# Kernel optimization log

Hardware: AMD Instinct MI355X
Metric: run time of the kernel (lower is better)

The kernel has to match this reference:

```python
import jax, jax.numpy as jnp
from jax import lax
import numpy as np

B, S, T = 32, 512, 64
IN, H, L, HC, OUT = 512, 512, 2, 4, 512

def setup_inputs() -> dict:
    key = jax.random.key(0)
    ks = jax.random.split(key, 12)
    def w(k, shape, fan_in):
        return (jax.random.normal(k, shape, jnp.float32) / np.float32(np.sqrt(fan_in)))
    lstm_in0 = IN + HC * H
    return {
        "inputs": jax.random.normal(ks[0], (B, T, IN), jnp.float32),
        "lengths": jax.random.randint(ks[1], (B,), 1, S + 1),
        "final_hiddens": jax.random.normal(ks[2], (L, B, H), jnp.float32),
        "hiddens": jax.random.normal(ks[3], (B, S, H), jnp.float32),
        "max_output_len": T,
        "max_seq_len": S,
        "Wa1": w(ks[4], (H, 2 * H), 2 * H), "ba1": jnp.zeros((H,), jnp.float32),
        "Wa2": w(ks[5], (HC, H), H), "ba2": jnp.zeros((HC,), jnp.float32),
        "W_ih0": w(ks[6], (4 * H, lstm_in0), lstm_in0), "W_hh0": w(ks[7], (4 * H, H), H),
        "b_ih0": jnp.zeros((4 * H,), jnp.float32), "b_hh0": jnp.zeros((4 * H,), jnp.float32),
        "W_ih1": w(ks[8], (4 * H, H), H), "W_hh1": w(ks[9], (4 * H, H), H),
        "b_ih1": jnp.zeros((4 * H,), jnp.float32), "b_hh1": jnp.zeros((4 * H,), jnp.float32),
        "Wo1": w(ks[10], (H, (1 + HC) * H), (1 + HC) * H), "bo1": jnp.zeros((H,), jnp.float32),
        "Wo2": w(ks[11], (OUT, H), H), "bo2": jnp.zeros((OUT,), jnp.float32),
    }

def _lstm_cell(x, h, c, W_ih, W_hh, b_ih, b_hh):
    # PyTorch LSTM gate order: i, f, g, o
    g = x @ W_ih.T + b_ih + h @ W_hh.T + b_hh
    i, f, gg, o = jnp.split(g, 4, axis=-1)
    c_new = jax.nn.sigmoid(f) * c + jax.nn.sigmoid(i) * jnp.tanh(gg)
    h_new = jax.nn.sigmoid(o) * jnp.tanh(c_new)
    return h_new, c_new

def reference(inputs, lengths, final_hiddens, hiddens, max_output_len, max_seq_len,
              Wa1, ba1, Wa2, ba2, W_ih0, W_hh0, b_ih0, b_hh0,
              W_ih1, W_hh1, b_ih1, b_hh1, Wo1, bo1, Wo2, bo2):
    batch = inputs.shape[0]
    # r_mask[b, s] = 1 if s < lengths[b] else 0  -> [B, S, 1]
    r_mask = (jnp.arange(max_seq_len)[None, :] < lengths[:, None]).astype(hiddens.dtype)[..., None]

    def step(carry, x_t):
        h, c = carry  # each [L, B, H]
        last = h[-1]  # [B, H]
        dup = last[:, None, :] * r_mask  # [B, S, H]
        a = jax.nn.relu(jnp.concatenate([dup, hiddens], axis=2) @ Wa1.T + ba1)  # [B,S,H]
        a = jax.nn.relu(a @ Wa2.T + ba2)  # [B,S,HC]
        a = jax.nn.softmax(a, axis=1)  # softmax over seq dim (unmasked, as in source)
        c_vecs = jnp.einsum('bsk,bsh->bkh', a, hiddens).reshape(batch, -1)  # [B, HC*H]
        x = jnp.concatenate([x_t, c_vecs], axis=1)  # [B, IN + HC*H]
        h0, c0 = _lstm_cell(x, h[0], c[0], W_ih0, W_hh0, b_ih0, b_hh0)
        h1, c1 = _lstm_cell(h0, h[1], c[1], W_ih1, W_hh1, b_ih1, b_hh1)
        out = jnp.tanh(jax.nn.relu(jnp.concatenate([h1, c_vecs], axis=1) @ Wo1.T + bo1) @ Wo2.T + bo2)
        return (jnp.stack([h0, h1]), jnp.stack([c0, c1])), out

    c_init = jnp.zeros_like(final_hiddens)
    _, outs = lax.scan(step, (final_hiddens, c_init), jnp.swapaxes(inputs, 0, 1))  # [T,B,OUT]
    return jnp.swapaxes(outs, 0, 1)  # [B, T, OUT]
```

## Files before the change

kernel.cpp:

```cpp
#include <hip/hip_runtime.h>
#include <cmath>


typedef unsigned short ushort;
typedef unsigned int uint;
typedef __attribute__((ext_vector_type(8))) short bf16x8;
typedef __attribute__((ext_vector_type(4))) float f32x4;

__device__ __forceinline__ float sigmoidf_(float x) { return 1.f / (1.f + __expf(-x)); }
__device__ __forceinline__ float bf2f(ushort u) {
  union { uint i; float f; } x; x.i = ((uint)u) << 16; return x.f;
}
__device__ __forceinline__ ushort f2bf(float f) {
  union { float f; uint i; } x; x.f = f;
  return (ushort)((x.i + 0x7FFFu + ((x.i >> 16) & 1u)) >> 16);
}
__device__ __forceinline__ float wave_sum(float v) {
#pragma unroll
  for (int m = 1; m < 64; m <<= 1) v += __shfl_xor(v, m, 64);
  return v;
}
__device__ __forceinline__ float wave_max(float v) {
#pragma unroll
  for (int m = 1; m < 64; m <<= 1) v = fmaxf(v, __shfl_xor(v, m, 64));
  return v;
}

__global__ void __launch_bounds__(256) k_init(const float* __restrict__ fh,
                                              ushort* h0b0, ushort* h1b0,
                                              float* c0, float* c1) {
  int i = blockIdx.x * 256 + threadIdx.x;
  h0b0[i] = f2bf(fh[i]);
  h1b0[i] = f2bf(fh[16384 + i]);
  c0[i] = 0.f; c1[i] = 0.f;
}

__global__ void __launch_bounds__(256) k_prep(const float* __restrict__ hid,
                                              ushort* __restrict__ hbf) {
  size_t i0 = ((size_t)blockIdx.x * 256 + threadIdx.x) * 8;
  float4 f0 = *(const float4*)&hid[i0];
  float4 f1 = *(const float4*)&hid[i0 + 4];
  uint4 o;
  o.x = (uint)f2bf(f0.x) | ((uint)f2bf(f0.y) << 16);
  o.y = (uint)f2bf(f0.z) | ((uint)f2bf(f0.w) << 16);
  o.z = (uint)f2bf(f1.x) | ((uint)f2bf(f1.y) << 16);
  o.w = (uint)f2bf(f1.z) | ((uint)f2bf(f1.w) << 16);
  *(uint4*)&hbf[i0] = o;
}

__global__ void __launch_bounds__(256) k_inprep(const float* __restrict__ inputs,
                                                ushort* __restrict__ inb) {
  size_t idx4 = ((size_t)blockIdx.x * 256 + threadIdx.x) * 4;
  int m = (int)(idx4 >> 9), k = (int)(idx4 & 511);
  int b = m & 31, tt = m >> 5;
  float4 v = *(const float4*)&inputs[((size_t)b * 64 + tt) * 512 + k];
  ushort4 o; o.x = f2bf(v.x); o.y = f2bf(v.y); o.z = f2bf(v.z); o.w = f2bf(v.w);
  *(ushort4*)&inb[(size_t)m * 512 + k] = o;
}

__global__ void __launch_bounds__(256) k_wcvt(const float* __restrict__ W1, int ld1,
                                              const float* __restrict__ W2, int ld2,
                                              int split, int K,
                                              ushort* __restrict__ dst) {
  size_t idx = ((size_t)blockIdx.x * 256 + threadIdx.x) * 4;
  int j = (int)(idx / K), k = (int)(idx % K);
  const float* src = (k < split) ? (W1 + (size_t)j * ld1 + k)
                                 : (W2 + (size_t)j * ld2 + (k - split));
  float4 v = *(const float4*)src;
  ushort4 o; o.x = f2bf(v.x); o.y = f2bf(v.y); o.z = f2bf(v.z); o.w = f2bf(v.w);
  *(ushort4*)&dst[idx] = o;
}

__device__ __forceinline__ void mfma_slice(
    const ushort* __restrict__ W, int ldW, int jrow0, int jstride,
    const ushort* __restrict__ xA, int ldA, int xsplit,
    const ushort* __restrict__ xB, int ldB, int coff,
    int klo, int khi, float* __restrict__ redrow) {
  const int l = threadIdx.x & 63;
  const int r16 = l & 15, koff = (l >> 4) * 8;
  const int j = jrow0 + (r16 & 3) + (r16 >> 2) * jstride;
  const ushort* wrow = W + (size_t)j * ldW + koff;
  const ushort* a0A = xA + (size_t)r16 * ldA + koff;
  const ushort* a1A = xA + (size_t)(16 + r16) * ldA + koff;
  const ushort* a0B = xB + (size_t)r16 * ldB + koff;
  const ushort* a1B = xB + (size_t)(16 + r16) * ldB + koff;
  f32x4 acc0 = {0.f, 0.f, 0.f, 0.f}, acc1 = {0.f, 0.f, 0.f, 0.f};
#pragma unroll 4
  for (int k0 = klo; k0 < khi; k0 += 32) {
    bf16x8 av0, av1;
    if (k0 < xsplit) {
      av0 = *(const bf16x8*)(a0A + k0);
      av1 = *(const bf16x8*)(a1A + k0);
    } else {
      av0 = *(const bf16x8*)(a0B + (k0 - coff));
      av1 = *(const bf16x8*)(a1B + (k0 - coff));
    }
    bf16x8 wv = *(const bf16x8*)(wrow + k0);
    acc0 = __builtin_amdgcn_mfma_f32_16x16x32_bf16(av0, wv, acc0, 0, 0, 0);
    acc1 = __builtin_amdgcn_mfma_f32_16x16x32_bf16(av1, wv, acc1, 0, 0, 0);
  }
  const int brow = (l >> 4) << 2;
#pragma unroll
  for (int r = 0; r < 4; r++) {
    redrow[r16 * 33 + brow + r] = acc0[r];
    redrow[r16 * 33 + 16 + brow + r] = acc1[r];
  }
}

__global__ void __launch_bounds__(256) k_hidproj2(const ushort* __restrict__ Wa1c,
                                                  const ushort* __restrict__ hbf,
                                                  ushort* __restrict__ hpb) {
  __shared__ float red[4 * 528];
  int tid = threadIdx.x, w = tid >> 6;
  int j0 = blockIdx.x * 16;
  for (int mt = 0; mt < 4; mt++) {
    int m0 = (blockIdx.y * 4 + mt) * 32;
    mfma_slice(Wa1c, 512, j0, 4, hbf + (size_t)m0 * 512, 512, 1 << 30,
               hbf + (size_t)m0 * 512, 512, 0, w * 128, w * 128 + 128,
               red + w * 528);
    __syncthreads();
#pragma unroll
    for (int e = 0; e < 2; e++) {
      int idx = tid + e * 256;
      int j = idx >> 5, b = idx & 31;
      float v = 0.f;
#pragma unroll
      for (int ww = 0; ww < 4; ww++) v += red[ww * 528 + j * 33 + b];
      hpb[(size_t)(m0 + b) * 512 + j0 + j] = f2bf(v);
    }
    __syncthreads();
  }
}

__global__ void __launch_bounds__(512) k_scst(const ushort* __restrict__ hpb,
                                              const float* __restrict__ ba1,
                                              const float* __restrict__ Wa2,
                                              float4* __restrict__ scoresP4) {
  __shared__ float wa2s[256], ba1s[64];
  int bid = blockIdx.x, tid = threadIdx.x;
  int b = bid >> 3, kdq = bid & 7, kd0 = kdq << 6, s = tid;
  if (tid < 256) wa2s[tid] = Wa2[(tid >> 6) * 512 + kd0 + (tid & 63)];
  else if (tid < 320) ba1s[tid - 256] = ba1[kd0 + (tid - 256)];
  __syncthreads();
  float a0 = 0.f, a1 = 0.f, a2 = 0.f, a3 = 0.f;
  const ushort* hpr = hpb + (size_t)(b * 512 + s) * 512 + kd0;
#pragma unroll
  for (int i8 = 0; i8 < 8; i8++) {
    bf16x8 hv8 = *(const bf16x8*)(hpr + i8 * 8);
#pragma unroll
    for (int e = 0; e < 8; e++) {
      int i = i8 * 8 + e;
      float a = fmaxf(bf2f(((ushort*)&hv8)[e]) + ba1s[i], 0.f);
      a0 += wa2s[i] * a;
      a1 += wa2s[64 + i] * a;
      a2 += wa2s[128 + i] * a;
      a3 += wa2s[192 + i] * a;
    }
  }
  scoresP4[((size_t)(kdq * 32 + b)) * 512 + s] = make_float4(a0, a1, a2, a3);
}

__global__ void __launch_bounds__(512) k_sum0(const float4* __restrict__ scoresP4,
                                              const float* __restrict__ ba2,
                                              float* __restrict__ scores0) {
  int idx = blockIdx.x * 512 + threadIdx.x;
  int b = idx >> 9, s = idx & 511;
  float a0 = ba2[0], a1 = ba2[1], a2 = ba2[2], a3 = ba2[3];
#pragma unroll
  for (int q = 0; q < 8; q++) {
    float4 p = scoresP4[((size_t)(q * 32 + b)) * 512 + s];
    a0 += p.x; a1 += p.y; a2 += p.z; a3 += p.w;
  }
  scores0[((size_t)b * 4 + 0) * 512 + s] = fmaxf(a0, 0.f);
  scores0[((size_t)b * 4 + 1) * 512 + s] = fmaxf(a1, 0.f);
  scores0[((size_t)b * 4 + 2) * 512 + s] = fmaxf(a2, 0.f);
  scores0[((size_t)b * 4 + 3) * 512 + s] = fmaxf(a3, 0.f);
}

__global__ void __launch_bounds__(512) k_stat0(const float* __restrict__ scores0,
                                               const int* __restrict__ lengths,
                                               float* __restrict__ m0v,
                                               float* __restrict__ statZ,
                                               float* __restrict__ P0) {
  __shared__ float st[32], st2[32];
  int b = blockIdx.x, tid = threadIdx.x, lane = tid & 63, w = tid >> 6;
  int s = tid, len = lengths[b];
  bool stat = s >= len;
  float v[4], m0[4];
#pragma unroll
  for (int k = 0; k < 4; k++) v[k] = scores0[((size_t)b * 4 + k) * 512 + s];
#pragma unroll
  for (int k = 0; k < 4; k++) {
    float mk = wave_max(stat ? v[k] : -1e30f);
    if (lane == 0) st[w * 4 + k] = mk;
  }
  __syncthreads();
#pragma unroll
  for (int k = 0; k < 4; k++) {
    float m = st[k];
#pragma unroll
    for (int w2 = 1; w2 < 8; w2++) m = fmaxf(m, st[w2 * 4 + k]);
    m0[k] = m;
  }
  float e[4];
#pragma unroll
  for (int k = 0; k < 4; k++) {
    e[k] = stat ? __expf(v[k] - m0[k]) : 0.f;
    float sk = wave_sum(e[k]);
    if (lane == 0) st2[w * 4 + k] = sk;
  }
  __syncthreads();
#pragma unroll
  for (int k = 0; k < 4; k++) {
    P0[((size_t)b * 4 + k) * 512 + s] = e[k];
  }
  if (tid == 0) {
#pragma unroll
    for (int k = 0; k < 4; k++) {
      float z = 0.f;
#pragma unroll
      for (int w2 = 0; w2 < 8; w2++) z += st2[w2 * 4 + k];
      m0v[b * 4 + k] = m0[k];
      statZ[b * 4 + k] = z;
    }
  }
}

__global__ void __launch_bounds__(512) k_statvec(const float* __restrict__ P0,
                                                 const ushort* __restrict__ hbf,
                                                 const int* __restrict__ lengths,
                                                 float* __restrict__ statvec) {
  __shared__ float P[4 * 512];
  __shared__ float red2[8 * 256];
  int bid = blockIdx.x, tid = threadIdx.x;
  int b = bid >> 3, hs = bid & 7;
#pragma unroll
  for (int k = 0; k < 4; k++) P[k * 512 + tid] = P0[((size_t)b * 4 + k) * 512 + tid];
  __syncthreads();
  int h = tid & 63, w8 = tid >> 6;
  int len = lengths[b];
  float a0 = 0.f, a1 = 0.f, a2 = 0.f, a3 = 0.f;
  for (int si = len + ((w8 - len) & 7); si < 512; si += 8) {
    float hv = bf2f(hbf[((size_t)(b * 512 + si) * 512) + (hs << 6) + h]);
    a0 += P[si] * hv;
    a1 += P[512 + si] * hv;
    a2 += P[1024 + si] * hv;
    a3 += P[1536 + si] * hv;
  }
  red2[(w8 << 8) + h] = a0;
  red2[(w8 << 8) + 64 + h] = a1;
  red2[(w8 << 8) + 128 + h] = a2;
  red2[(w8 << 8) + 192 + h] = a3;
  __syncthreads();
  if (tid < 256) {
    int k = tid >> 6, hh = tid & 63;
    float acc = 0.f;
#pragma unroll
    for (int c = 0; c < 8; c++) acc += red2[(c << 8) + (k << 6) + hh];
    statvec[((size_t)b * 4 + k) * 512 + (hs << 6) + hh] = acc;
  }
}

__global__ void __launch_bounds__(256) k_gin0(const ushort* __restrict__ Wg0b,
                                              const ushort* __restrict__ inb,
                                              float* __restrict__ gi0) {
  __shared__ float red[4 * 528];
  int tid = threadIdx.x, w = tid >> 6;
  int j0 = blockIdx.x * 16;
  for (int mt = 0; mt < 4; mt++) {
    int m0 = (blockIdx.y * 4 + mt) * 32;
    mfma_slice(Wg0b, 3072, j0, 4, inb + (size_t)m0 * 512, 512, 1 << 30,
               inb + (size_t)m0 * 512, 512, 0, w * 128, w * 128 + 128,
               red + w * 528);
    __syncthreads();
#pragma unroll
    for (int e = 0; e < 2; e++) {
      int idx = tid + e * 256;
      int j = idx >> 5, b = idx & 31;
      float v = 0.f;
#pragma unroll
      for (int ww = 0; ww < 4; ww++) v += red[ww * 528 + j * 33 + b];
      gi0[(size_t)(m0 + b) * 2048 + j0 + j] = v;
    }
    __syncthreads();
  }
}

__global__ void __launch_bounds__(512) k_scq(
    const ushort* __restrict__ Wq, const ushort* __restrict__ Wo1,
    const ushort* __restrict__ h1cur, const ushort* __restrict__ xb,
    const float* __restrict__ bo1, ushort* __restrict__ o1bf,
    const ushort* __restrict__ hpb, const float* __restrict__ ba1,
    const float* __restrict__ Wa2, const int* __restrict__ lengths,
    float4* __restrict__ scoresP4, int t) {
  __shared__ float red[8 * 528];
  __shared__ float qs[64], wa2s[256], ba1s[64];
  int bid = blockIdx.x, tid = threadIdx.x, w = tid >> 6, lane = tid & 63;
  if (bid < 32) {
    if (t < 1) return;
    mfma_slice(Wo1, 2560, bid * 16, 4, h1cur, 512, 512, xb, 2048, 512,
               w * 320, w * 320 + 320, red + w * 528);
    __syncthreads();
    int j = tid & 15, b = tid >> 4;
    float v = 0.f;
#pragma unroll
    for (int ww = 0; ww < 8; ww++) v += red[ww * 528 + j * 33 + b];
    int jj = bid * 16 + j;
    o1bf[b * 512 + jj] = f2bf(fmaxf(v + bo1[jj], 0.f));
  } else {
    if (t >= 64) return;
    int r = bid - 32;
    int b = r >> 3, kdq = r & 7, kd0 = kdq << 6;
    if (tid < 256) wa2s[tid] = Wa2[(tid >> 6) * 512 + kd0 + (tid & 63)];
    else if (tid < 320) ba1s[tid - 256] = ba1[kd0 + (tid - 256)];
    {
      bf16x8 hv8 = *(const bf16x8*)(h1cur + b * 512 + lane * 8);
      float hf[8];
#pragma unroll
      for (int e2 = 0; e2 < 8; e2++) hf[e2] = bf2f(((ushort*)&hv8)[e2]);
#pragma unroll
      for (int rr = 0; rr < 8; rr++) {
        int row = kd0 + w * 8 + rr;
        bf16x8 wv8 = *(const bf16x8*)(Wq + (size_t)row * 512 + lane * 8);
        float acc = 0.f;
#pragma unroll
        for (int e2 = 0; e2 < 8; e2++) acc += hf[e2] * bf2f(((ushort*)&wv8)[e2]);
        acc = wave_sum(acc);
        if (lane == 0) qs[w * 8 + rr] = acc;
      }
    }
    __syncthreads();
    int s = tid, len = lengths[b];
    if ((tid & ~63) >= len) return;
    float m = (s < len) ? 1.f : 0.f;
    float a0 = 0.f, a1 = 0.f, a2 = 0.f, a3 = 0.f;
    const ushort* hpr = hpb + (size_t)(b * 512 + s) * 512 + kd0;
#pragma unroll
    for (int i8 = 0; i8 < 8; i8++) {
      bf16x8 hv8 = *(const bf16x8*)(hpr + i8 * 8);
#pragma unroll
      for (int e = 0; e < 8; e++) {
        int i = i8 * 8 + e;
        float a = fmaxf(bf2f(((ushort*)&hv8)[e]) + ba1s[i] + m * qs[i], 0.f);
        a0 += wa2s[i] * a;
        a1 += wa2s[64 + i] * a;
        a2 += wa2s[128 + i] * a;
        a3 += wa2s[192 + i] * a;
      }
    }
    scoresP4[((size_t)(kdq * 32 + b)) * 512 + s] = make_float4(a0, a1, a2, a3);
  }
}

__global__ void __launch_bounds__(512) k_ctxout(
    const float4* __restrict__ scoresP4, const float* __restrict__ ba2,
    const int* __restrict__ lengths, const ushort* __restrict__ hbf,
    const float* __restrict__ m0v, const float* __restrict__ statZ,
    const float* __restrict__ statvec, ushort* __restrict__ xb,
    const ushort* __restrict__ Wo2, const ushort* __restrict__ o1bf,
    const float* __restrict__ bo2, float* __restrict__ outp, int t) {
  __shared__ float red[8 * 528];
  __shared__ float P[4 * 512];
  __shared__ float red2[8 * 256];
  __shared__ float st[32], st2[32];
  int bid = blockIdx.x, tid = threadIdx.x;
  if (bid < 32) {
    if (t < 1) return;
    int w = tid >> 6;
    mfma_slice(Wo2, 512, bid * 16, 4, o1bf, 512, 1 << 30, o1bf, 512, 0,
               w * 64, w * 64 + 64, red + w * 528);
    __syncthreads();
    int j = tid & 15, b = tid >> 4;
    float v = 0.f;
#pragma unroll
    for (int ww = 0; ww < 8; ww++) v += red[ww * 528 + j * 33 + b];
    int jj = bid * 16 + j;
    outp[((size_t)b * 64 + (t - 1)) * 512 + jj] = tanhf(v + bo2[jj]);
  } else {
    if (t >= 64) return;
    int r = bid - 32;
    int b = r >> 3, hs = r & 7;
    int lane = tid & 63, w = tid >> 6;
    int s = tid, len = lengths[b];
    bool act = s < len;
    float v[4];
    {
      float a0 = ba2[0], a1 = ba2[1], a2 = ba2[2], a3 = ba2[3];
      if (act) {
#pragma unroll
        for (int q = 0; q < 8; q++) {
          float4 p = scoresP4[((size_t)(q * 32 + b)) * 512 + s];
          a0 += p.x; a1 += p.y; a2 += p.z; a3 += p.w;
        }
        v[0] = fmaxf(a0, 0.f); v[1] = fmaxf(a1, 0.f);
        v[2] = fmaxf(a2, 0.f); v[3] = fmaxf(a3, 0.f);
      } else {
        v[0] = v[1] = v[2] = v[3] = -1e30f;
      }
    }
    float M[4];
#pragma unroll
    for (int k = 0; k < 4; k++) {
      float mk = wave_max(v[k]);
      if (lane == 0) st[w * 4 + k] = mk;
    }
    __syncthreads();
#pragma unroll
    for (int k = 0; k < 4; k++) {
      float m = st[k];
#pragma unroll
      for (int w2 = 1; w2 < 8; w2++) m = fmaxf(m, st[w2 * 4 + k]);
      M[k] = fmaxf(m, m0v[b * 4 + k]);
    }
    float e[4];
#pragma unroll
    for (int k = 0; k < 4; k++) {
      e[k] = act ? __expf(v[k] - M[k]) : 0.f;
      float sk = wave_sum(e[k]);
      if (lane == 0) st2[w * 4 + k] = sk;
    }
    __syncthreads();
    float sc[4];
#pragma unroll
    for (int k = 0; k < 4; k++) {
      float dynZ = 0.f;
#pragma unroll
      for (int w2 = 0; w2 < 8; w2++) dynZ += st2[w2 * 4 + k];
      float scB = __expf(m0v[b * 4 + k] - M[k]);
      float Z = dynZ + scB * statZ[b * 4 + k];
      float invZ = 1.f / Z;
      P[k * 512 + s] = e[k] * invZ;
      sc[k] = scB * invZ;
    }
    __syncthreads();
    int h = tid & 63, w8 = tid >> 6;
    float a0 = 0.f, a1 = 0.f, a2 = 0.f, a3 = 0.f;
    const ushort* hb0 = hbf + ((size_t)b * 512) * 512 + (hs << 6) + h;
    int si = w8;
    for (; si + 24 < len; si += 32) {
      float h0v = bf2f(hb0[(size_t)si * 512]);
      float h1v = bf2f(hb0[(size_t)(si + 8) * 512]);
      float h2v = bf2f(hb0[(size_t)(si + 16) * 512]);
      float h3v = bf2f(hb0[(size_t)(si + 24) * 512]);
      a0 += P[si] * h0v + P[si + 8] * h1v + P[si + 16] * h2v + P[si + 24] * h3v;
      a1 += P[512 + si] * h0v + P[512 + si + 8] * h1v + P[512 + si + 16] * h2v +
            P[512 + si + 24] * h3v;
      a2 += P[1024 + si] * h0v + P[1024 + si + 8] * h1v + P[1024 + si + 16] * h2v +
            P[1024 + si + 24] * h3v;
      a3 += P[1536 + si] * h0v + P[1536 + si + 8] * h1v + P[1536 + si + 16] * h2v +
            P[1536 + si + 24] * h3v;
    }
    for (; si < len; si += 8) {
      float hv = bf2f(hb0[(size_t)si * 512]);
      a0 += P[si] * hv;
      a1 += P[512 + si] * hv;
      a2 += P[1024 + si] * hv;
      a3 += P[1536 + si] * hv;
    }
    red2[(w8 << 8) + h] = a0;
    red2[(w8 << 8) + 64 + h] = a1;
    red2[(w8 << 8) + 128 + h] = a2;
    red2[(w8 << 8) + 192 + h] = a3;
    __syncthreads();
    if (tid < 256) {
      int k = tid >> 6, hh = tid & 63;
      float acc = 0.f;
#pragma unroll
      for (int c = 0; c < 8; c++) acc += red2[(c << 8) + (k << 6) + hh];
      acc += sc[k] * statvec[((size_t)b * 4 + k) * 512 + (hs << 6) + hh];
      xb[b * 2048 + (k << 9) + (hs << 6) + hh] = f2bf(acc);
    }
  }
}

__global__ void __launch_bounds__(512) k_cell0(
    const ushort* __restrict__ Wg0b, const ushort* __restrict__ xb,
    const ushort* __restrict__ h0cur, const float* __restrict__ gi0,
    const float* __restrict__ bih, const float* __restrict__ bhh,
    float* __restrict__ cst, ushort* __restrict__ hnew, int t) {
  __shared__ float red[8 * 528];
  int bid = blockIdx.x, tid = threadIdx.x, w = tid >> 6;
  mfma_slice(Wg0b + 512, 3072, bid * 4, 512, xb, 2048, 2048, h0cur, 512, 2048,
             w * 320, w * 320 + 320, red + w * 528);
  __syncthreads();
  if (tid < 128) {
    int b = tid & 31, dh = tid >> 5;
    int h = bid * 4 + dh;
    float G[4];
#pragma unroll
    for (int g = 0; g < 4; g++) {
      float v = bih[g * 512 + h] + bhh[g * 512 + h] +
                gi0[(size_t)(t * 32 + b) * 2048 + g * 512 + h];
#pragma unroll
      for (int ww = 0; ww < 8; ww++) v += red[ww * 528 + (g * 4 + dh) * 33 + b];
      G[g] = v;
    }
    float i_ = sigmoidf_(G[0]), f_ = sigmoidf_(G[1]);
    float gg = tanhf(G[2]), o_ = sigmoidf_(G[3]);
    float cn = f_ * cst[b * 512 + h] + i_ * gg;
    cst[b * 512 + h] = cn;
    hnew[b * 512 + h] = f2bf(o_ * tanhf(cn));
  }
}

__global__ void __launch_bounds__(512) k_cell1(
    const ushort* __restrict__ Wg1b, const ushort* __restrict__ h0new,
    const ushort* __restrict__ h1cur, const float* __restrict__ bih,
    const float* __restrict__ bhh, float* __restrict__ cst,
    ushort* __restrict__ hnew) {
  __shared__ float red[8 * 528];
  int bid = blockIdx.x, tid = threadIdx.x, w = tid >> 6;
  mfma_slice(Wg1b, 1024, bid * 4, 512, h0new, 512, 512, h1cur, 512, 512,
             w * 128, w * 128 + 128, red + w * 528);
  __syncthreads();
  if (tid < 128) {
    int b = tid & 31, dh = tid >> 5;
    int h = bid * 4 + dh;
    float G[4];
#pragma unroll
    for (int g = 0; g < 4; g++) {
      float v = bih[g * 512 + h] + bhh[g * 512 + h];
#pragma unroll
      for (int ww = 0; ww < 8; ww++) v += red[ww * 528 + (g * 4 + dh) * 33 + b];
      G[g] = v;
    }
    float i_ = sigmoidf_(G[0]), f_ = sigmoidf_(G[1]);
    float gg = tanhf(G[2]), o_ = sigmoidf_(G[3]);
    float cn = f_ * cst[b * 512 + h] + i_ * gg;
    cst[b * 512 + h] = cn;
    hnew[b * 512 + h] = f2bf(o_ * tanhf(cn));
  }
}

extern "C" void kernel_launch(void* const* d_in, const int* in_sizes, int n_in,
                              void* d_out, int out_size, void* d_ws, size_t ws_size,
                              hipStream_t stream) {
  const float* inputs  = (const float*)d_in[0];
  const int*   lengths = (const int*)d_in[1];
  const float* fh      = (const float*)d_in[2];
  const float* hiddens = (const float*)d_in[3];
  const float* Wa1  = (const float*)d_in[6];
  const float* ba1  = (const float*)d_in[7];
  const float* Wa2  = (const float*)d_in[8];
  const float* ba2  = (const float*)d_in[9];
  const float* Wih0 = (const float*)d_in[10];
  const float* Whh0 = (const float*)d_in[11];
  const float* bih0 = (const float*)d_in[12];
  const float* bhh0 = (const float*)d_in[13];
  const float* Wih1 = (const float*)d_in[14];
  const float* Whh1 = (const float*)d_in[15];
  const float* bih1 = (const float*)d_in[16];
  const float* bhh1 = (const float*)d_in[17];
  const float* Wo1  = (const float*)d_in[18];
  const float* bo1  = (const float*)d_in[19];
  const float* Wo2  = (const float*)d_in[20];
  const float* bo2  = (const float*)d_in[21];
  float* outp = (float*)d_out;

  char* p = (char*)d_ws;
  ushort* hpb = (ushort*)p; p += (size_t)32 * 512 * 512 * 2;
  ushort* hbf = (ushort*)p; p += (size_t)32 * 512 * 512 * 2;
  float4* scoresP4 = (float4*)p; p += (size_t)8 * 32 * 512 * 16;
  float* scores0 = (float*)p; p += (size_t)32 * 4 * 512 * 4;
  float* P0      = (float*)p; p += (size_t)32 * 4 * 512 * 4;
  float* statvec = (float*)p; p += (size_t)32 * 4 * 512 * 4;
  float* m0v     = (float*)p; p += 128 * sizeof(float);
  float* statZ   = (float*)p; p += 128 * sizeof(float);
  ushort* xb     = (ushort*)p; p += (size_t)32 * 2048 * 2;
  ushort* h0b    = (ushort*)p; p += (size_t)2 * 32 * 512 * 2;
  ushort* h1b    = (ushort*)p; p += (size_t)2 * 32 * 512 * 2;
  ushort* o1bf   = (ushort*)p; p += (size_t)32 * 512 * 2;
  float* c0      = (float*)p; p += (size_t)32 * 512 * 4;
  float* c1      = (float*)p; p += (size_t)32 * 512 * 4;
  ushort* Wg0b   = (ushort*)p; p += (size_t)2048 * 3072 * 2;
  ushort* Wg1b   = (ushort*)p; p += (size_t)2048 * 1024 * 2;
  ushort* Wo1b   = (ushort*)p; p += (size_t)512 * 2560 * 2;
  ushort* Wo2b   = (ushort*)p; p += (size_t)512 * 512 * 2;
  ushort* Wqb    = (ushort*)p; p += (size_t)512 * 512 * 2;
  ushort* Wa1c   = (ushort*)p; p += (size_t)512 * 512 * 2;
  ushort* inb    = (ushort*)p; p += (size_t)2048 * 512 * 2;
  float* gi0     = (float*)p; p += (size_t)2048 * 2048 * 4;

  k_init<<<64, 256, 0, stream>>>(fh, h0b, h1b, c0, c1);
  k_prep<<<4096, 256, 0, stream>>>(hiddens, hbf);
  k_inprep<<<1024, 256, 0, stream>>>(inputs, inb);
  k_wcvt<<<6144, 256, 0, stream>>>(Wih0, 2560, Whh0, 512, 2560, 3072, Wg0b);
  k_wcvt<<<2048, 256, 0, stream>>>(Wih1, 512, Whh1, 512, 512, 1024, Wg1b);
  k_wcvt<<<1280, 256, 0, stream>>>(Wo1, 2560, Wo1, 2560, 2560, 2560, Wo1b);
  k_wcvt<<<256, 256, 0, stream>>>(Wo2, 512, Wo2, 512, 512, 512, Wo2b);
  k_wcvt<<<256, 256, 0, stream>>>(Wa1, 1024, Wa1, 1024, 512, 512, Wqb);
  k_wcvt<<<256, 256, 0, stream>>>(Wa1 + 512, 1024, Wa1 + 512, 1024, 1 << 30, 512, Wa1c);
  k_hidproj2<<<dim3(32, 128), 256, 0, stream>>>(Wa1c, hbf, hpb);
  k_gin0<<<dim3(128, 16), 256, 0, stream>>>(Wg0b, inb, gi0);
  k_scst<<<256, 512, 0, stream>>>(hpb, ba1, Wa2, scoresP4);
  k_sum0<<<32, 512, 0, stream>>>(scoresP4, ba2, scores0);
  k_stat0<<<32, 512, 0, stream>>>(scores0, lengths, m0v, statZ, P0);
  k_statvec<<<256, 512, 0, stream>>>(P0, hbf, lengths, statvec);

  for (int t = 0; t <= 64; t++) {
    const ushort* h1cur = h1b + (size_t)(t & 1) * 16384;
    const ushort* h0cur = h0b + (size_t)(t & 1) * 16384;
    ushort* h0nxt = h0b + (size_t)((t + 1) & 1) * 16384;
    ushort* h1nxt = h1b + (size_t)((t + 1) & 1) * 16384;
    k_scq<<<288, 512, 0, stream>>>(Wqb, Wo1b, h1cur, xb, bo1, o1bf, hpb, ba1,
                                   Wa2, lengths, scoresP4, t);
    k_ctxout<<<288, 512, 0, stream>>>(scoresP4, ba2, lengths, hbf, m0v, statZ,
                                      statvec, xb, Wo2b, o1bf, bo2, outp, t);
    if (t < 64) {
      k_cell0<<<128, 512, 0, stream>>>(Wg0b, xb, h0cur, gi0, bih0, bhh0, c0,
                                       h0nxt, t);
      k_cell1<<<128, 512, 0, stream>>>(Wg1b, h0nxt, h1cur, bih1, bhh1, c1, h1nxt);
    }
  }
}
```

Before: 2.913 ms.

## Precompute recurrent h@W_hh gate terms in earlier kernels to shorten cell critical path

The recurrent W_hh·h contributions for both LSTM layers are moved out of the cell kernels. They now run as extra blocks in k_scq (layer 1) and k_ctxout (layer 0), which already have h available, and are written to gh0/gh1 buffers that the cell kernels read. This shrinks the serial GEMM work inside k_cell0/k_cell1. Separately, the attention score partitioning changes from 8 to 4 slices of 128 features, which halves the partial-sum traffic but doubles the per-block work. The extra blocks add launch width and global round-trips for the gate partials.

```diff
diff --git a/kernel.cpp b/kernel.cpp
--- a/kernel.cpp
+++ b/kernel.cpp
@@ -136,25 +136,25 @@
                                               const float* __restrict__ ba1,
                                               const float* __restrict__ Wa2,
                                               float4* __restrict__ scoresP4) {
-  __shared__ float wa2s[256], ba1s[64];
+  __shared__ float wa2s[512], ba1s[128];
   int bid = blockIdx.x, tid = threadIdx.x;
-  int b = bid >> 3, kdq = bid & 7, kd0 = kdq << 6, s = tid;
-  if (tid < 256) wa2s[tid] = Wa2[(tid >> 6) * 512 + kd0 + (tid & 63)];
-  else if (tid < 320) ba1s[tid - 256] = ba1[kd0 + (tid - 256)];
+  int b = bid >> 2, kdq = bid & 3, kd0 = kdq << 7, s = tid;
+  wa2s[tid] = Wa2[(tid >> 7) * 512 + kd0 + (tid & 127)];
+  if (tid < 128) ba1s[tid] = ba1[kd0 + tid];
   __syncthreads();
   float a0 = 0.f, a1 = 0.f, a2 = 0.f, a3 = 0.f;
   const ushort* hpr = hpb + (size_t)(b * 512 + s) * 512 + kd0;
 #pragma unroll
-  for (int i8 = 0; i8 < 8; i8++) {
+  for (int i8 = 0; i8 < 16; i8++) {
     bf16x8 hv8 = *(const bf16x8*)(hpr + i8 * 8);
 #pragma unroll
     for (int e = 0; e < 8; e++) {
       int i = i8 * 8 + e;
       float a = fmaxf(bf2f(((ushort*)&hv8)[e]) + ba1s[i], 0.f);
       a0 += wa2s[i] * a;
-      a1 += wa2s[64 + i] * a;
-      a2 += wa2s[128 + i] * a;
-      a3 += wa2s[192 + i] * a;
+      a1 += wa2s[128 + i] * a;
+      a2 += wa2s[256 + i] * a;
+      a3 += wa2s[384 + i] * a;
     }
   }
   scoresP4[((size_t)(kdq * 32 + b)) * 512 + s] = make_float4(a0, a1, a2, a3);
@@ -167,7 +167,7 @@
   int b = idx >> 9, s = idx & 511;
   float a0 = ba2[0], a1 = ba2[1], a2 = ba2[2], a3 = ba2[3];
 #pragma unroll
-  for (int q = 0; q < 8; q++) {
+  for (int q = 0; q < 4; q++) {
     float4 p = scoresP4[((size_t)(q * 32 + b)) * 512 + s];
     a0 += p.x; a1 += p.y; a2 += p.z; a3 += p.w;
   }
@@ -292,9 +292,10 @@
     const float* __restrict__ bo1, ushort* __restrict__ o1bf,
     const ushort* __restrict__ hpb, const float* __restrict__ ba1,
     const float* __restrict__ Wa2, const int* __restrict__ lengths,
-    float4* __restrict__ scoresP4, int t) {
+    float4* __restrict__ scoresP4, const ushort* __restrict__ Wg1b,
+    float* __restrict__ gh1, int t) {
   __shared__ float red[8 * 528];
-  __shared__ float qs[64], wa2s[256], ba1s[64];
+  __shared__ float qs[128], wa2s[512], ba1s[128];
   int bid = blockIdx.x, tid = threadIdx.x, w = tid >> 6, lane = tid & 63;
   if (bid < 32) {
     if (t < 1) return;
@@ -307,26 +308,26 @@
     for (int ww = 0; ww < 8; ww++) v += red[ww * 528 + j * 33 + b];
     int jj = bid * 16 + j;
     o1bf[b * 512 + jj] = f2bf(fmaxf(v + bo1[jj], 0.f));
-  } else {
+  } else if (bid < 160) {
     if (t >= 64) return;
     int r = bid - 32;
-    int b = r >> 3, kdq = r & 7, kd0 = kdq << 6;
-    if (tid < 256) wa2s[tid] = Wa2[(tid >> 6) * 512 + kd0 + (tid & 63)];
-    else if (tid < 320) ba1s[tid - 256] = ba1[kd0 + (tid - 256)];
+    int b = r >> 2, kdq = r & 3, kd0 = kdq << 7;
+    wa2s[tid] = Wa2[(tid >> 7) * 512 + kd0 + (tid & 127)];
+    if (tid < 128) ba1s[tid] = ba1[kd0 + tid];
     {
       bf16x8 hv8 = *(const bf16x8*)(h1cur + b * 512 + lane * 8);
       float hf[8];
 #pragma unroll
       for (int e2 = 0; e2 < 8; e2++) hf[e2] = bf2f(((ushort*)&hv8)[e2]);
 #pragma unroll
-      for (int rr = 0; rr < 8; rr++) {
-        int row = kd0 + w * 8 + rr;
+      for (int rr = 0; rr < 16; rr++) {
+        int row = kd0 + w * 16 + rr;
         bf16x8 wv8 = *(const bf16x8*)(Wq + (size_t)row * 512 + lane * 8);
         float acc = 0.f;
 #pragma unroll
         for (int e2 = 0; e2 < 8; e2++) acc += hf[e2] * bf2f(((ushort*)&wv8)[e2]);
         acc = wave_sum(acc);
-        if (lane == 0) qs[w * 8 + rr] = acc;
+        if (lane == 0) qs[w * 16 + rr] = acc;
       }
     }
     __syncthreads();
@@ -336,19 +337,31 @@
     float a0 = 0.f, a1 = 0.f, a2 = 0.f, a3 = 0.f;
     const ushort* hpr = hpb + (size_t)(b * 512 + s) * 512 + kd0;
 #pragma unroll
-    for (int i8 = 0; i8 < 8; i8++) {
+    for (int i8 = 0; i8 < 16; i8++) {
       bf16x8 hv8 = *(const bf16x8*)(hpr + i8 * 8);
 #pragma unroll
       for (int e = 0; e < 8; e++) {
         int i = i8 * 8 + e;
         float a = fmaxf(bf2f(((ushort*)&hv8)[e]) + ba1s[i] + m * qs[i], 0.f);
         a0 += wa2s[i] * a;
-        a1 += wa2s[64 + i] * a;
-        a2 += wa2s[128 + i] * a;
-        a3 += wa2s[192 + i] * a;
+        a1 += wa2s[128 + i] * a;
+        a2 += wa2s[256 + i] * a;
+        a3 += wa2s[384 + i] * a;
       }
     }
     scoresP4[((size_t)(kdq * 32 + b)) * 512 + s] = make_float4(a0, a1, a2, a3);
+  } else {
+    if (t >= 64) return;
+    int bid2 = bid - 160;
+    mfma_slice(Wg1b + 512, 1024, bid2 * 4, 512, h1cur, 512, 1 << 30, h1cur, 512,
+               0, w * 64, w * 64 + 64, red + w * 528);
+    __syncthreads();
+    int r16 = tid >> 5, b = tid & 31;
+    float v = 0.f;
+#pragma unroll
+    for (int ww = 0; ww < 8; ww++) v += red[ww * 528 + r16 * 33 + b];
+    int j = (r16 >> 2) * 512 + bid2 * 4 + (r16 & 3);
+    gh1[(size_t)j * 32 + b] = v;
   }
 }
 
@@ -358,7 +371,9 @@
     const float* __restrict__ m0v, const float* __restrict__ statZ,
     const float* __restrict__ statvec, ushort* __restrict__ xb,
     const ushort* __restrict__ Wo2, const ushort* __restrict__ o1bf,
-    const float* __restrict__ bo2, float* __restrict__ outp, int t) {
+    const float* __restrict__ bo2, float* __restrict__ outp,
+    const ushort* __restrict__ Wg0b, const ushort* __restrict__ h0cur,
+    float* __restrict__ gh0, int t) {
   __shared__ float red[8 * 528];
   __shared__ float P[4 * 512];
   __shared__ float red2[8 * 256];
@@ -376,7 +391,7 @@
     for (int ww = 0; ww < 8; ww++) v += red[ww * 528 + j * 33 + b];
     int jj = bid * 16 + j;
     outp[((size_t)b * 64 + (t - 1)) * 512 + jj] = tanhf(v + bo2[jj]);
-  } else {
+  } else if (bid < 288) {
     if (t >= 64) return;
     int r = bid - 32;
     int b = r >> 3, hs = r & 7;
@@ -388,7 +403,7 @@
       float a0 = ba2[0], a1 = ba2[1], a2 = ba2[2], a3 = ba2[3];
       if (act) {
 #pragma unroll
-        for (int q = 0; q < 8; q++) {
+        for (int q = 0; q < 4; q++) {
           float4 p = scoresP4[((size_t)(q * 32 + b)) * 512 + s];
           a0 += p.x; a1 += p.y; a2 += p.z; a3 += p.w;
         }
@@ -470,18 +485,31 @@
       acc += sc[k] * statvec[((size_t)b * 4 + k) * 512 + (hs << 6) + hh];
       xb[b * 2048 + (k << 9) + (hs << 6) + hh] = f2bf(acc);
     }
+  } else {
+    if (t >= 64) return;
+    int bid3 = bid - 288;
+    int w = tid >> 6;
+    mfma_slice(Wg0b + 2560, 3072, bid3 * 4, 512, h0cur, 512, 1 << 30, h0cur,
+               512, 0, w * 64, w * 64 + 64, red + w * 528);
+    __syncthreads();
+    int r16 = tid >> 5, b = tid & 31;
+    float v = 0.f;
+#pragma unroll
+    for (int ww = 0; ww < 8; ww++) v += red[ww * 528 + r16 * 33 + b];
+    int j = (r16 >> 2) * 512 + bid3 * 4 + (r16 & 3);
+    gh0[(size_t)j * 32 + b] = v;
   }
 }
 
 __global__ void __launch_bounds__(512) k_cell0(
     const ushort* __restrict__ Wg0b, const ushort* __restrict__ xb,
-    const ushort* __restrict__ h0cur, const float* __restrict__ gi0,
+    const float* __restrict__ gh0, const float* __restrict__ gi0,
     const float* __restrict__ bih, const float* __restrict__ bhh,
     float* __restrict__ cst, ushort* __restrict__ hnew, int t) {
   __shared__ float red[8 * 528];
   int bid = blockIdx.x, tid = threadIdx.x, w = tid >> 6;
-  mfma_slice(Wg0b + 512, 3072, bid * 4, 512, xb, 2048, 2048, h0cur, 512, 2048,
-             w * 320, w * 320 + 320, red + w * 528);
+  mfma_slice(Wg0b + 512, 3072, bid * 4, 512, xb, 2048, 1 << 30, xb, 2048, 0,
+             w * 256, w * 256 + 256, red + w * 528);
   __syncthreads();
   if (tid < 128) {
     int b = tid & 31, dh = tid >> 5;
@@ -489,8 +517,9 @@
     float G[4];
 #pragma unroll
     for (int g = 0; g < 4; g++) {
-      float v = bih[g * 512 + h] + bhh[g * 512 + h] +
-                gi0[(size_t)(t * 32 + b) * 2048 + g * 512 + h];
+      int j = g * 512 + h;
+      float v = bih[j] + bhh[j] + gi0[(size_t)(t * 32 + b) * 2048 + j] +
+                gh0[(size_t)j * 32 + b];
 #pragma unroll
       for (int ww = 0; ww < 8; ww++) v += red[ww * 528 + (g * 4 + dh) * 33 + b];
       G[g] = v;
@@ -505,13 +534,13 @@
 
 __global__ void __launch_bounds__(512) k_cell1(
     const ushort* __restrict__ Wg1b, const ushort* __restrict__ h0new,
-    const ushort* __restrict__ h1cur, const float* __restrict__ bih,
+    const float* __restrict__ gh1, const float* __restrict__ bih,
     const float* __restrict__ bhh, float* __restrict__ cst,
     ushort* __restrict__ hnew) {
   __shared__ float red[8 * 528];
   int bid = blockIdx.x, tid = threadIdx.x, w = tid >> 6;
-  mfma_slice(Wg1b, 1024, bid * 4, 512, h0new, 512, 512, h1cur, 512, 512,
-             w * 128, w * 128 + 128, red + w * 528);
+  mfma_slice(Wg1b, 1024, bid * 4, 512, h0new, 512, 1 << 30, h0new, 512, 0,
+             w * 64, w * 64 + 64, red + w * 528);
   __syncthreads();
   if (tid < 128) {
     int b = tid & 31, dh = tid >> 5;
@@ -519,7 +548,8 @@
     float G[4];
 #pragma unroll
     for (int g = 0; g < 4; g++) {
-      float v = bih[g * 512 + h] + bhh[g * 512 + h];
+      int j = g * 512 + h;
+      float v = bih[j] + bhh[j] + gh1[(size_t)j * 32 + b];
 #pragma unroll
       for (int ww = 0; ww < 8; ww++) v += red[ww * 528 + (g * 4 + dh) * 33 + b];
       G[g] = v;
@@ -560,12 +590,14 @@
   char* p = (char*)d_ws;
   ushort* hpb = (ushort*)p; p += (size_t)32 * 512 * 512 * 2;
   ushort* hbf = (ushort*)p; p += (size_t)32 * 512 * 512 * 2;
-  float4* scoresP4 = (float4*)p; p += (size_t)8 * 32 * 512 * 16;
+  float4* scoresP4 = (float4*)p; p += (size_t)4 * 32 * 512 * 16;
   float* scores0 = (float*)p; p += (size_t)32 * 4 * 512 * 4;
   float* P0      = (float*)p; p += (size_t)32 * 4 * 512 * 4;
   float* statvec = (float*)p; p += (size_t)32 * 4 * 512 * 4;
   float* m0v     = (float*)p; p += 128 * sizeof(float);
   float* statZ   = (float*)p; p += 128 * sizeof(float);
+  float* gh0     = (float*)p; p += (size_t)2048 * 32 * 4;
+  float* gh1     = (float*)p; p += (size_t)2048 * 32 * 4;
   ushort* xb     = (ushort*)p; p += (size_t)32 * 2048 * 2;
   ushort* h0b    = (ushort*)p; p += (size_t)2 * 32 * 512 * 2;
   ushort* h1b    = (ushort*)p; p += (size_t)2 * 32 * 512 * 2;
@@ -592,7 +624,7 @@
   k_wcvt<<<256, 256, 0, stream>>>(Wa1 + 512, 1024, Wa1 + 512, 1024, 1 << 30, 512, Wa1c);
   k_hidproj2<<<dim3(32, 128), 256, 0, stream>>>(Wa1c, hbf, hpb);
   k_gin0<<<dim3(128, 16), 256, 0, stream>>>(Wg0b, inb, gi0);
-  k_scst<<<256, 512, 0, stream>>>(hpb, ba1, Wa2, scoresP4);
+  k_scst<<<128, 512, 0, stream>>>(hpb, ba1, Wa2, scoresP4);
   k_sum0<<<32, 512, 0, stream>>>(scoresP4, ba2, scores0);
   k_stat0<<<32, 512, 0, stream>>>(scores0, lengths, m0v, statZ, P0);
   k_statvec<<<256, 512, 0, stream>>>(P0, hbf, lengths, statvec);
@@ -603,13 +635,14 @@
     ushort* h0nxt = h0b + (size_t)((t + 1) & 1) * 16384;
     ushort* h1nxt = h1b + (size_t)((t + 1) & 1) * 16384;
     k_scq<<<288, 512, 0, stream>>>(Wqb, Wo1b, h1cur, xb, bo1, o1bf, hpb, ba1,
-                                   Wa2, lengths, scoresP4, t);
-    k_ctxout<<<288, 512, 0, stream>>>(scoresP4, ba2, lengths, hbf, m0v, statZ,
-                                      statvec, xb, Wo2b, o1bf, bo2, outp, t);
+                                   Wa2, lengths, scoresP4, Wg1b, gh1, t);
+    k_ctxout<<<416, 512, 0, stream>>>(scoresP4, ba2, lengths, hbf, m0v, statZ,
+                                      statvec, xb, Wo2b, o1bf, bo2, outp,
+                                      Wg0b, h0cur, gh0, t);
     if (t < 64) {
-      k_cell0<<<128, 512, 0, stream>>>(Wg0b, xb, h0cur, gi0, bih0, bhh0, c0,
+      k_cell0<<<128, 512, 0, stream>>>(Wg0b, xb, gh0, gi0, bih0, bhh0, c0,
                                        h0nxt, t);
-      k_cell1<<<128, 512, 0, stream>>>(Wg1b, h0nxt, h1cur, bih1, bhh1, c1, h1nxt);
-    }
-  }
-}
+      k_cell1<<<128, 512, 0, stream>>>(Wg1b, h0nxt, gh1, bih1, bhh1, c1, h1nxt);
+    }
+  }
+}
```

Result: slower. 3.011 ms (+3.4%).
